# Optimization experiments

Hardware: AMD Instinct MI355X
Metric: run time of the kernel (lower is better)

Reference implementation:

```python
import jax, jax.numpy as jnp
import numpy as np

N = 16384
K = 8

def knn_indices(pos, k):
    # squared pairwise distances via ||a||^2 + ||b||^2 - 2 a.b  -> [N, N]
    sq = jnp.sum(pos * pos, axis=-1)
    d = sq[:, None] + sq[None, :] - 2.0 * (pos @ pos.T)
    n = pos.shape[0]
    d = d.at[jnp.arange(n), jnp.arange(n)].set(jnp.inf)  # exclude self (loop=False)
    _, idx = jax.lax.top_k(-d, k)  # k nearest neighbors per target node
    # PointNetConv adds self-loops by default -> append self index
    return jnp.concatenate([idx, jnp.arange(n)[:, None]], axis=1)  # [N, k+1]

def mlp(x, W1, b1, W2, b2):
    return jax.nn.relu(x @ W1 + b1) @ W2 + b2

def pointnet_conv(x, pos, idx, W1, b1, W2, b2):
    # message: concat(x_j, pos_j - pos_i); aggregate: max over neighbors
    rel = pos[idx] - pos[:, None, :]                 # [N, k+1, 3]
    msg = jnp.concatenate([x[idx], rel], axis=-1)    # [N, k+1, d+3]
    h = mlp(msg, W1, b1, W2, b2)                     # [N, k+1, d_out]
    return jnp.max(h, axis=1)                        # [N, d_out]

def setup_inputs() -> dict:
    key = jax.random.key(0)
    ks = jax.random.split(key, 11)
    def lin(k, fi, fo):
        kw, kb = jax.random.split(k)
        s = 1.0 / np.sqrt(fi)
        return (jax.random.uniform(kw, (fi, fo), jnp.float32, -s, s),
                jax.random.uniform(kb, (fo,), jnp.float32, -s, s))
    W1a, b1a = lin(ks[0], 6, 32)
    W1b, b1b = lin(ks[1], 32, 64)
    W2a, b2a = lin(ks[2], 67, 64)
    W2b, b2b = lin(ks[3], 64, 128)
    Wc, bc = lin(ks[4], 128, 5)
    pos = jax.random.normal(ks[5], (N, 3), jnp.float32)
    return {"pos": pos, "W1a": W1a, "b1a": b1a, "W1b": W1b, "b1b": b1b,
            "W2a": W2a, "b2a": b2a, "W2b": W2b, "b2b": b2b, "Wc": Wc, "bc": bc}

def reference(pos, W1a, b1a, W1b, b1b, W2a, b2a, W2b, b2b, Wc, bc):
    idx = knn_indices(pos, K)                                    # [N, K+1]
    x = jax.nn.relu(pointnet_conv(pos, pos, idx, W1a, b1a, W1b, b1b))  # [N, 64]
    x = jax.nn.relu(pointnet_conv(x, pos, idx, W2a, b2a, W2b, b2b))    # [N, 128]
    logits = x @ Wc + bc                                         # [N, 5]
    return jax.nn.log_softmax(logits, axis=-1)
```

## Files before the change

### kernel.cpp

```cpp
#include <hip/hip_runtime.h>
#include <hip/hip_bf16.h>
#include <math.h>

#define N_PTS 16384
#define KNN 8

#define DT_BF16 1
#define DT_FP32 2

#define WS_FLAG_OFF 0
#define WS_IDX_OFF  64
#define WS_X1_OFF   589888
#define WS_NEEDED   4784192

#define WS_SAT_OFF      (WS_X1_OFF)
#define WS_START_OFF    (WS_X1_OFF + 442368)
#define WS_CURSOR_OFF   (WS_X1_OFF + 884800)
#define WS_PID_OFF      (WS_X1_OFF + 1327168)
#define WS_PTS_OFF      (WS_X1_OFF + 1392704)
#define WS_ROWTOT_OFF   (WS_X1_OFF + 1654848)
#define WS_ROWSTART_OFF (WS_X1_OFF + 1664064)

#define GRID_R   48
#define NROWS2D  (GRID_R * GRID_R)
#define NCELLS   (GRID_R * GRID_R * GRID_R)
#define GLO      -4.5f
#define CELL_E   0.1875f
#define CELL_INV 5.3333335f
#define NBR_MIN  26

__device__ __forceinline__ float bf2f(__hip_bfloat16 v) { return __bfloat162float(v); }

__device__ __forceinline__ float ldf(const float* p, int i) { return p[i]; }
__device__ __forceinline__ float ldf(const __hip_bfloat16* p, int i) { return bf2f(p[i]); }
__device__ __forceinline__ void stf(float* p, int i, float v) { p[i] = v; }
__device__ __forceinline__ void stf(__hip_bfloat16* p, int i, float v) { p[i] = __float2bfloat16(v); }

__device__ __forceinline__ int clamp_idx(int j) {
    return ((unsigned)j < (unsigned)N_PTS) ? j : 0;
}

__device__ __forceinline__ int cell_of(float v) {
    int c = (int)((v - GLO) * CELL_INV);
    return min(max(c, 0), GRID_R - 1);
}

__device__ __forceinline__ int get_dt(const int* flag) {
    return (flag[0] > 16) ? DT_FP32 : DT_BF16;
}

__global__ __launch_bounds__(256) void zero_kernel(int* __restrict__ cnt, int* __restrict__ flag) {
    const int e = blockIdx.x * 256 + threadIdx.x;
    cnt[e] = 0;
    if (e == 0) flag[0] = 0;
}

__global__ __launch_bounds__(256) void sniff_kernel(const unsigned short* __restrict__ posu,
                                                    int* __restrict__ flag) {
    __shared__ int red[256];
    int local = 0;
    for (int e = blockIdx.x * 256 + threadIdx.x; e < 3 * N_PTS; e += 64 * 256) {
        const float v = __uint_as_float(((unsigned)posu[e]) << 16);
        if (!(fabsf(v) <= 64.0f)) local++;
    }
    red[threadIdx.x] = local;
    __syncthreads();
    for (int s = 128; s > 0; s >>= 1) {
        if (threadIdx.x < s) red[threadIdx.x] += red[threadIdx.x + s];
        __syncthreads();
    }
    if (threadIdx.x == 0 && red[0] > 0) atomicAdd(flag, red[0]);
}

template <typename T>
__device__ __forceinline__ void count_body(const T* __restrict__ pos, int* __restrict__ cnt) {
    const int i = blockIdx.x * 256 + threadIdx.x;
    const float x = ldf(pos, 3 * i + 0);
    const float y = ldf(pos, 3 * i + 1);
    const float z = ldf(pos, 3 * i + 2);
    const int c = (cell_of(z) * GRID_R + cell_of(y)) * GRID_R + cell_of(x);
    atomicAdd(&cnt[c], 1);
}

__global__ __launch_bounds__(256) void grid_count_kernel(const void* __restrict__ pos,
                                                         const int* __restrict__ flag,
                                                         int* __restrict__ cnt) {
    if (get_dt(flag) == DT_BF16) count_body<__hip_bfloat16>((const __hip_bfloat16*)pos, cnt);
    else                         count_body<float>((const float*)pos, cnt);
}

__global__ __launch_bounds__(256) void rowscan_kernel(int* __restrict__ sat,
                                                      int* __restrict__ rowtot) {
    const int t = blockIdx.x * 256 + threadIdx.x;
    const int rb = t * GRID_R;
    int acc = 0;
    for (int x = 0; x < GRID_R; ++x) { acc += sat[rb + x]; sat[rb + x] = acc; }
    rowtot[t] = acc;
}

__global__ __launch_bounds__(256) void rowoffset_kernel(const int* __restrict__ rowtot,
                                                        int* __restrict__ rowstart) {
    __shared__ int part[256];
    const int t = threadIdx.x;
    int loc[9]; int s = 0;
#pragma unroll
    for (int k = 0; k < 9; ++k) { loc[k] = rowtot[t * 9 + k]; s += loc[k]; }
    part[t] = s;
    __syncthreads();
    for (int off = 1; off < 256; off <<= 1) {
        int v = (t >= off) ? part[t - off] : 0;
        __syncthreads();
        part[t] += v;
        __syncthreads();
    }
    int run = (t == 0) ? 0 : part[t - 1];
#pragma unroll
    for (int k = 0; k < 9; ++k) { rowstart[t * 9 + k] = run; run += loc[k]; }
}

__global__ __launch_bounds__(256) void cellstart_kernel(const int* __restrict__ satx,
                                                        const int* __restrict__ rowstart,
                                                        int* __restrict__ cstart,
                                                        int* __restrict__ cursor) {
    const int t = blockIdx.x * 256 + threadIdx.x;
    const int rb = t * GRID_R;
    const int base = rowstart[t];
    int prev = 0;
    for (int x = 0; x < GRID_R; ++x) {
        const int v = base + prev;
        cstart[rb + x] = v;
        cursor[rb + x] = v;
        prev = satx[rb + x];
    }
    if (t == NROWS2D - 1) cstart[NCELLS] = base + prev;
}

__global__ __launch_bounds__(256) void saty_kernel(int* __restrict__ sat) {
    const int t = blockIdx.x * 256 + threadIdx.x;
    const int z = t / GRID_R, x = t - z * GRID_R;
    const int base = z * NROWS2D + x;
    int run = 0;
#pragma unroll
    for (int y = 0; y < GRID_R; ++y) {
        run += sat[base + y * GRID_R];
        sat[base + y * GRID_R] = run;
    }
}

__global__ __launch_bounds__(256) void satz_kernel(int* __restrict__ sat) {
    const int t = blockIdx.x * 256 + threadIdx.x;
    int run = 0;
#pragma unroll
    for (int z = 0; z < GRID_R; ++z) {
        run += sat[t + z * NROWS2D];
        sat[t + z * NROWS2D] = run;
    }
}

template <typename T>
__device__ __forceinline__ void scatter_body(const T* __restrict__ pos, int* __restrict__ cursor,
                                             float4* __restrict__ pts4, int* __restrict__ pid) {
    const int i = blockIdx.x * 256 + threadIdx.x;
    const float x = ldf(pos, 3 * i + 0);
    const float y = ldf(pos, 3 * i + 1);
    const float z = ldf(pos, 3 * i + 2);
    const int c = (cell_of(z) * GRID_R + cell_of(y)) * GRID_R + cell_of(x);
    const int slot = atomicAdd(&cursor[c], 1);
    const float sq = fmaf(x, x, fmaf(y, y, z * z));
    pts4[slot] = make_float4(-2.0f * x, -2.0f * y, -2.0f * z, sq);
    pid[slot] = i;
}

__global__ __launch_bounds__(256) void grid_scatter_kernel(const void* __restrict__ pos,
                                                           const int* __restrict__ flag,
                                                           int* __restrict__ cursor,
                                                           float4* __restrict__ pts4,
                                                           int* __restrict__ pid) {
    if (get_dt(flag) == DT_BF16) scatter_body<__hip_bfloat16>((const __hip_bfloat16*)pos, cursor, pts4, pid);
    else                         scatter_body<float>((const float*)pos, cursor, pts4, pid);
}

__device__ __forceinline__ int sat_at(const int* __restrict__ sat, int x, int y, int z) {
    if (x < 0 || y < 0 || z < 0) return 0;
    return sat[(z * GRID_R + y) * GRID_R + x];
}

__device__ __forceinline__ int boxcount(const int* __restrict__ sat,
                                        int x0, int x1, int y0, int y1, int z0, int z1) {
    return sat_at(sat, x1, y1, z1) - sat_at(sat, x0 - 1, y1, z1)
         - sat_at(sat, x1, y0 - 1, z1) - sat_at(sat, x1, y1, z0 - 1)
         + sat_at(sat, x0 - 1, y0 - 1, z1) + sat_at(sat, x0 - 1, y1, z0 - 1)
         + sat_at(sat, x1, y0 - 1, z0 - 1) - sat_at(sat, x0 - 1, y0 - 1, z0 - 1);
}

template <typename T>
__device__ void knn_body(const T* __restrict__ pos,
                         const int* __restrict__ cstart, const int* __restrict__ sat,
                         const float4* __restrict__ pts4, const int* __restrict__ pid,
                         int* __restrict__ idx_out,
                         int* __restrict__ rs, int* __restrict__ epf) {
    const int tid  = threadIdx.x;
    const int lane = tid & 31;
    const int i    = blockIdx.x * 8 + (tid >> 5);

    const float pix = ldf(pos, 3 * i + 0);
    const float piy = ldf(pos, 3 * i + 1);
    const float piz = ldf(pos, 3 * i + 2);
    const float sqi = fmaf(pix, pix, fmaf(piy, piy, piz * piz));
    const int cx = cell_of(pix), cy = cell_of(piy), cz = cell_of(piz);

    float bd[KNN];
    int   bi[KNN];
#pragma unroll
    for (int q = 0; q < KNN; ++q) { bd[q] = INFINITY; bi[q] = 0x7fffffff; }
    float tau = INFINITY;

    auto do_insert = [&](float d, int pj) {
        float cd = d; int ci = pj;
#pragma unroll
        for (int q = 0; q < KNN; ++q) {
            const bool ins = (cd < bd[q]) || (cd == bd[q] && ci < bi[q]);
            const float nd = ins ? cd : bd[q];
            const int   ni = ins ? ci : bi[q];
            const float od = ins ? bd[q] : cd;
            const int   oi = ins ? bi[q] : ci;
            bd[q] = nd; bi[q] = ni; cd = od; ci = oi;
        }
        tau = fminf(tau, bd[KNN - 1]);
    };

    auto scan_win = [&](int rr) {
        const int x0 = max(cx - rr, 0), x1 = min(cx + rr, GRID_R - 1);
        const int y0 = max(cy - rr, 0), y1 = min(cy + rr, GRID_R - 1);
        const int z0 = max(cz - rr, 0), z1 = min(cz + rr, GRID_R - 1);
        const int ny = y1 - y0 + 1;
        const int R  = ny * (z1 - z0 + 1);
        const int xs = x1 - x0 + 1;
        for (int cb = 0; cb < R; cb += 32) {
            const int lr = cb + lane;
            int cnt_r = 0, st_r = 0;
            if (lr < R) {
                const int iz = lr / ny;
                const int iy = lr - iz * ny;
                const int c0 = ((z0 + iz) * GRID_R + (y0 + iy)) * GRID_R + x0;
                st_r  = cstart[c0];
                cnt_r = cstart[c0 + xs] - st_r;
            }
            int pv = cnt_r;
#pragma unroll
            for (int s = 1; s < 32; s <<= 1) {
                const int u = __shfl_up(pv, s, 32);
                if (lane >= s) pv += u;
            }
            const int Mtot = __shfl(pv, 31, 32);
            asm volatile("s_waitcnt lgkmcnt(0)" ::: "memory");
            rs[lane]  = st_r;
            epf[lane] = (lr < R) ? (pv - cnt_r) : 0x7fffffff;
            asm volatile("s_waitcnt lgkmcnt(0)" ::: "memory");
            for (int tb = 0; tb < Mtot; tb += 128) {
                float dls[4]; int pjs[4];
#pragma unroll
                for (int k = 0; k < 4; ++k) {
                    const int t = tb + (k << 5) + lane;
                    dls[k] = INFINITY; pjs[k] = i;
                    if (t < Mtot) {
                        int p = 0;
#pragma unroll
                        for (int st = 16; st >= 1; st >>= 1)
                            if (epf[p + st] <= t) p += st;
                        const int si = rs[p] + (t - epf[p]);
                        const float4 cq = pts4[si];
                        pjs[k] = pid[si];
                        dls[k] = fmaf(cq.x, pix, fmaf(cq.y, piy, fmaf(cq.z, piz, cq.w)));
                    }
                }
#pragma unroll
                for (int k = 0; k < 4; ++k)
                    if (pjs[k] != i && dls[k] <= tau) do_insert(dls[k], pjs[k]);
            }
        }
    };

    float od[KNN];
    int   oi[KNN];
    auto merge_out = [&]() {
#pragma unroll
        for (int k = 0; k < KNN; ++k) {
            float dw = bd[0];
            int   iw = bi[0];
#pragma unroll
            for (int s = 1; s < 32; s <<= 1) {
                const float dx = __shfl_xor(dw, s, 32);
                const int   ix = __shfl_xor(iw, s, 32);
                if (dx < dw || (dx == dw && ix < iw)) { dw = dx; iw = ix; }
            }
            if (bd[0] == dw && bi[0] == iw) {
#pragma unroll
                for (int q = 0; q < KNN - 1; ++q) { bd[q] = bd[q + 1]; bi[q] = bi[q + 1]; }
                bd[KNN - 1] = INFINITY; bi[KNN - 1] = 0x7fffffff;
            }
            od[k] = dw; oi[k] = iw;
        }
    };

    int r;
    {
        const int rl = lane + 1;
        const int bx0 = max(cx - rl, 0), bx1 = min(cx + rl, GRID_R - 1);
        const int by0 = max(cy - rl, 0), by1 = min(cy + rl, GRID_R - 1);
        const int bz0 = max(cz - rl, 0), bz1 = min(cz + rl, GRID_R - 1);
        const int cntl = boxcount(sat, bx0, bx1, by0, by1, bz0, bz1);
        const unsigned long long m = __ballot(cntl >= NBR_MIN);
        const unsigned mh = (unsigned)(m >> (tid & 32));
        r = mh ? (int)__ffs(mh) : 32;
    }

    scan_win(r);

    {
        float mg = INFINITY;
        bool full = true;
        if (cx - r > 0)          { mg = fminf(mg, pix - (GLO + (float)(cx - r) * CELL_E));     full = false; }
        if (cx + r < GRID_R - 1) { mg = fminf(mg, (GLO + (float)(cx + r + 1) * CELL_E) - pix); full = false; }
        if (cy - r > 0)          { mg = fminf(mg, piy - (GLO + (float)(cy - r) * CELL_E));     full = false; }
        if (cy + r < GRID_R - 1) { mg = fminf(mg, (GLO + (float)(cy + r + 1) * CELL_E) - piy); full = false; }
        if (cz - r > 0)          { mg = fminf(mg, piz - (GLO + (float)(cz - r) * CELL_E));     full = false; }
        if (cz + r < GRID_R - 1) { mg = fminf(mg, (GLO + (float)(cz + r + 1) * CELL_E) - piz); full = false; }

        merge_out();
        bool done = full;
        const float d8 = od[KNN - 1];
        if (!full) {
            const float mge  = mg - 1e-5f;
            const float need = mge * mge - sqi;
            done = (d8 < need);
        }

        if (!done) {
            float s2 = sqrtf(fmaxf(d8 + sqi, 0.0f)) + 1e-4f;
            s2 = fminf(s2, 9.0f);
            auto dneed = [&](float frac, int clip) -> int {
                int nd = (int)ceilf((s2 - frac) * CELL_INV);
                nd = max(nd, 0);
                return min(nd, clip);
            };
            const float fxm = pix - (GLO + (float)cx * CELL_E);
            const float fxp = (GLO + (float)(cx + 1) * CELL_E) - pix;
            const float fym = piy - (GLO + (float)cy * CELL_E);
            const float fyp = (GLO + (float)(cy + 1) * CELL_E) - piy;
            const float fzm = piz - (GLO + (float)cz * CELL_E);
            const float fzp = (GLO + (float)(cz + 1) * CELL_E) - piz;
            int r2 = r + 1;
            r2 = max(r2, dneed(fxm, cx));
            r2 = max(r2, dneed(fxp, GRID_R - 1 - cx));
            r2 = max(r2, dneed(fym, cy));
            r2 = max(r2, dneed(fyp, GRID_R - 1 - cy));
            r2 = max(r2, dneed(fzm, cz));
            r2 = max(r2, dneed(fzp, GRID_R - 1 - cz));
            r2 = min(r2, GRID_R);

#pragma unroll
            for (int q = 0; q < KNN; ++q) { bd[q] = INFINITY; bi[q] = 0x7fffffff; }
            tau = d8;
            scan_win(r2);
            merge_out();
        }
    }

    if (lane == 0) {
#pragma unroll
        for (int k = 0; k < KNN; ++k) idx_out[i * 9 + k] = clamp_idx(oi[k]);
        idx_out[i * 9 + 8] = i;
    }
}

__global__ __launch_bounds__(256) void knn_grid_kernel(const void* __restrict__ pos,
                                                       const int* __restrict__ flag,
                                                       const int* __restrict__ cstart,
                                                       const int* __restrict__ sat,
                                                       const float4* __restrict__ pts4,
                                                       const int* __restrict__ pid,
                                                       int* __restrict__ idx_out) {
    __shared__ int rs[8][32];
    __shared__ int epf[8][32];
    const int sg = threadIdx.x >> 5;
    if (get_dt(flag) == DT_BF16)
        knn_body<__hip_bfloat16>((const __hip_bfloat16*)pos, cstart, sat, pts4, pid, idx_out,
                                 rs[sg], epf[sg]);
    else
        knn_body<float>((const float*)pos, cstart, sat, pts4, pid, idx_out, rs[sg], epf[sg]);
}

struct Conv1Smem {
    alignas(16) float wB[32 * 64];
    alignas(16) float h1s[4][9 * 32];
    alignas(16) float wsum[3 * 32];
    alignas(16) float wbot[3 * 32];
    alignas(16) float posn[4][9][3];
    float bA[32];
    float bB[64];
};

template <typename T>
__device__ void conv1_body(const T* __restrict__ pos, const int* __restrict__ idx,
                           const T* __restrict__ W1a, const T* __restrict__ b1a,
                           const T* __restrict__ W1b, const T* __restrict__ b1b,
                           float* __restrict__ x1, Conv1Smem& s) {
    const int tid = threadIdx.x;
    for (int e = tid; e < 96; e += 256) {
        const float bot = ldf(W1a, 96 + e);
        s.wsum[e] = ldf(W1a, e) + bot;
        s.wbot[e] = bot;
    }
    if (tid < 32) s.bA[tid] = ldf(b1a, tid);
    for (int e = tid; e < 2048; e += 256) s.wB[e] = ldf(W1b, e);
    if (tid < 64) s.bB[tid] = ldf(b1b, tid);

    const int tl   = tid >> 6;
    const int lane = tid & 63;
    const int i    = blockIdx.x * 4 + tl;

    if (lane < 27) {
        const int n = lane / 3, c = lane % 3;
        const int j = clamp_idx(idx[i * 9 + n]);
        s.posn[tl][n][c] = ldf(pos, 3 * j + c);
    }
    const float pi0 = ldf(pos, 3 * i + 0);
    const float pi1 = ldf(pos, 3 * i + 1);
    const float pi2 = ldf(pos, 3 * i + 2);
    __syncthreads();

    for (int e = lane; e < 288; e += 64) {
        const int n = e >> 5, k = e & 31;
        float b = fmaf(pi0, s.wbot[k], fmaf(pi1, s.wbot[32 + k], pi2 * s.wbot[64 + k]));
        float v = s.bA[k] - b;
        v = fmaf(s.posn[tl][n][0], s.wsum[k], v);
        v = fmaf(s.posn[tl][n][1], s.wsum[32 + k], v);
        v = fmaf(s.posn[tl][n][2], s.wsum[64 + k], v);
        s.h1s[tl][n * 32 + k] = fmaxf(v, 0.0f);
    }
    __syncthreads();

    float wcol[32];
#pragma unroll
    for (int k = 0; k < 32; ++k) wcol[k] = s.wB[k * 64 + lane];

    float acc = -INFINITY;
    for (int n = 0; n < 9; ++n) {
        float v = s.bB[lane];
#pragma unroll
        for (int k = 0; k < 32; ++k) v = fmaf(s.h1s[tl][n * 32 + k], wcol[k], v);
        acc = fmaxf(acc, v);
    }
    x1[i * 64 + lane] = fmaxf(acc, 0.0f);
}

__global__ __launch_bounds__(256) void conv1_kernel(const void* __restrict__ pos,
                                                    const int* __restrict__ flag,
                                                    const int* __restrict__ idx,
                                                    const void* __restrict__ W1a,
                                                    const void* __restrict__ b1a,
                                                    const void* __restrict__ W1b,
                                                    const void* __restrict__ b1b,
                                                    float* __restrict__ x1) {
    __shared__ Conv1Smem s;
    if (get_dt(flag) == DT_BF16)
        conv1_body<__hip_bfloat16>((const __hip_bfloat16*)pos, idx,
            (const __hip_bfloat16*)W1a, (const __hip_bfloat16*)b1a,
            (const __hip_bfloat16*)W1b, (const __hip_bfloat16*)b1b, x1, s);
    else
        conv1_body<float>((const float*)pos, idx, (const float*)W1a, (const float*)b1a,
            (const float*)W1b, (const float*)b1b, x1, s);
}

struct ZwSmem {
    alignas(16) float wA[67 * 64];
    alignas(16) float xrT[4][68][4];
    float bA[64];
};

template <typename T>
__device__ void zw_body(const T* __restrict__ pos, const T* __restrict__ W2a,
                        const T* __restrict__ b2a, float* __restrict__ x1, ZwSmem& s) {
    const int tid  = threadIdx.x;
    const int wv   = tid >> 6;
    const int lane = tid & 63;
    const int j0   = blockIdx.x * 16 + wv * 4;

    for (int e = tid; e < 4288; e += 256) s.wA[e] = ldf(W2a, e);
    if (tid < 64) s.bA[tid] = ldf(b2a, tid);

#pragma unroll
    for (int p = 0; p < 4; ++p)
        s.xrT[wv][lane][p] = x1[(j0 + p) * 64 + lane];
    if (lane < 12) {
        const int p = lane / 3, c = lane % 3;
        s.xrT[wv][64 + c][p] = ldf(pos, 3 * (j0 + p) + c);
    }
    __syncthreads();

    float a0 = s.bA[lane], a1 = a0, a2 = a0, a3 = a0;
    for (int c = 0; c < 67; ++c) {
        const float w = s.wA[c * 64 + lane];
        const float4 xv = *(const float4*)&s.xrT[wv][c][0];
        a0 = fmaf(xv.x, w, a0);
        a1 = fmaf(xv.y, w, a1);
        a2 = fmaf(xv.z, w, a2);
        a3 = fmaf(xv.w, w, a3);
    }
    x1[(j0 + 0) * 64 + lane] = a0;
    x1[(j0 + 1) * 64 + lane] = a1;
    x1[(j0 + 2) * 64 + lane] = a2;
    x1[(j0 + 3) * 64 + lane] = a3;
}

__global__ __launch_bounds__(256) void zw_kernel(const void* __restrict__ pos,
                                                 const int* __restrict__ flag,
                                                 const void* __restrict__ W2a,
                                                 const void* __restrict__ b2a,
                                                 float* __restrict__ x1) {
    __shared__ ZwSmem s;
    if (get_dt(flag) == DT_BF16)
        zw_body<__hip_bfloat16>((const __hip_bfloat16*)pos, (const __hip_bfloat16*)W2a,
                                (const __hip_bfloat16*)b2a, x1, s);
    else
        zw_body<float>((const float*)pos, (const float*)W2a, (const float*)b2a, x1, s);
}

struct Conv2Smem {
    alignas(16) float h1s[4][9 * 64];
    alignas(16) float row[4][128];
    alignas(16) float wbot[3 * 64];
    alignas(16) float wc[640];
    float bcs[5];
    float sv[4][5];
    int   nb[4][9];
};

template <typename T>
__device__ void conv2_body(const T* __restrict__ pos, const int* __restrict__ idx,
                           const float* __restrict__ zw,
                           const T* __restrict__ W2a, const T* __restrict__ W2b,
                           const T* __restrict__ b2b, const T* __restrict__ Wc,
                           const T* __restrict__ bc, T* __restrict__ out, Conv2Smem& s) {
    const int tid  = threadIdx.x;
    const int l    = tid & 127;
    const int half = tid >> 7;

    float wcol[64];
#pragma unroll
    for (int k = 0; k < 64; ++k) wcol[k] = ldf(W2b, k * 128 + l);
    const float bBl = ldf(b2b, l);

    for (int e = tid; e < 192; e += 256) s.wbot[e] = ldf(W2a, 4096 + e);
    for (int e = tid; e < 640; e += 256) s.wc[e] = ldf(Wc, e);
    if (tid < 5) s.bcs[tid] = ldf(bc, tid);

    const int tl   = tid >> 6;
    const int lane = tid & 63;
    const int i    = blockIdx.x * 4 + tl;

    if (lane < 9) s.nb[tl][lane] = clamp_idx(idx[i * 9 + lane]);
    const float pi0 = ldf(pos, 3 * i + 0);
    const float pi1 = ldf(pos, 3 * i + 1);
    const float pi2 = ldf(pos, 3 * i + 2);
    __syncthreads();

    {
        const float vi = fmaf(pi0, s.wbot[lane], fmaf(pi1, s.wbot[64 + lane], pi2 * s.wbot[128 + lane]));
#pragma unroll
        for (int n = 0; n < 9; ++n) {
            const int j = s.nb[tl][n];
            s.h1s[tl][n * 64 + lane] = fmaxf(zw[j * 64 + lane] - vi, 0.0f);
        }
    }
    __syncthreads();

#pragma unroll
    for (int tt = 0; tt < 2; ++tt) {
        const int tgt = half * 2 + tt;
        float acc = -INFINITY;
        for (int n = 0; n < 9; ++n) {
            float v = bBl;
            for (int k = 0; k < 64; k += 4) {
                const float4 hv = *(const float4*)&s.h1s[tgt][n * 64 + k];
                v = fmaf(hv.x, wcol[k + 0], v);
                v = fmaf(hv.y, wcol[k + 1], v);
                v = fmaf(hv.z, wcol[k + 2], v);
                v = fmaf(hv.w, wcol[k + 3], v);
            }
            acc = fmaxf(acc, v);
        }
        s.row[tgt][l] = fmaxf(acc, 0.0f);
    }
    __syncthreads();

    if (tid < 20) {
        const int tgt = tid / 5, o = tid % 5;
        float v = s.bcs[o];
        for (int k = 0; k < 128; ++k) v = fmaf(s.row[tgt][k], s.wc[k * 5 + o], v);
        s.sv[tgt][o] = v;
    }
    __syncthreads();
    if (tid < 20) {
        const int tgt = tid / 5, o = tid % 5;
        float m = s.sv[tgt][0];
#pragma unroll
        for (int q = 1; q < 5; ++q) m = fmaxf(m, s.sv[tgt][q]);
        float sum = 0.0f;
#pragma unroll
        for (int q = 0; q < 5; ++q) sum += expf(s.sv[tgt][q] - m);
        const float lse = m + logf(sum);
        stf(out, (blockIdx.x * 4 + tgt) * 5 + o, s.sv[tgt][o] - lse);
    }
}

__global__ __launch_bounds__(256) void conv2_head_kernel(const void* __restrict__ pos,
                                                         const int* __restrict__ flag,
                                                         const int* __restrict__ idx,
                                                         const float* __restrict__ zw,
                                                         const void* __restrict__ W2a,
                                                         const void* __restrict__ W2b,
                                                         const void* __restrict__ b2b,
                                                         const void* __restrict__ Wc,
                                                         const void* __restrict__ bc,
                                                         void* __restrict__ out) {
    __shared__ Conv2Smem s;
    if (get_dt(flag) == DT_BF16)
        conv2_body<__hip_bfloat16>((const __hip_bfloat16*)pos, idx, zw,
            (const __hip_bfloat16*)W2a, (const __hip_bfloat16*)W2b, (const __hip_bfloat16*)b2b,
            (const __hip_bfloat16*)Wc, (const __hip_bfloat16*)bc, (__hip_bfloat16*)out, s);
    else
        conv2_body<float>((const float*)pos, idx, zw, (const float*)W2a, (const float*)W2b,
            (const float*)b2b, (const float*)Wc, (const float*)bc, (float*)out, s);
}

extern "C" void kernel_launch(void* const* d_in, const int* in_sizes, int n_in,
                              void* d_out, int out_size, void* d_ws, size_t ws_size,
                              hipStream_t stream) {
    if (ws_size < (size_t)WS_NEEDED) return;

    char* ws = (char*)d_ws;
    int*    flag     = (int*)(ws + WS_FLAG_OFF);
    int*    idx      = (int*)(ws + WS_IDX_OFF);
    float*  x1       = (float*)(ws + WS_X1_OFF);
    int*    sat      = (int*)(ws + WS_SAT_OFF);
    int*    cstart   = (int*)(ws + WS_START_OFF);
    int*    cursor   = (int*)(ws + WS_CURSOR_OFF);
    int*    pid      = (int*)(ws + WS_PID_OFF);
    float4* pts4     = (float4*)(ws + WS_PTS_OFF);
    int*    rowtot   = (int*)(ws + WS_ROWTOT_OFF);
    int*    rowstart = (int*)(ws + WS_ROWSTART_OFF);

    zero_kernel<<<NCELLS / 256, 256, 0, stream>>>(sat, flag);
    sniff_kernel<<<64, 256, 0, stream>>>((const unsigned short*)d_in[0], flag);
    grid_count_kernel<<<N_PTS / 256, 256, 0, stream>>>(d_in[0], flag, sat);
    rowscan_kernel<<<NROWS2D / 256, 256, 0, stream>>>(sat, rowtot);
    rowoffset_kernel<<<1, 256, 0, stream>>>(rowtot, rowstart);
    cellstart_kernel<<<NROWS2D / 256, 256, 0, stream>>>(sat, rowstart, cstart, cursor);
    saty_kernel<<<NROWS2D / 256, 256, 0, stream>>>(sat);
    satz_kernel<<<NROWS2D / 256, 256, 0, stream>>>(sat);
    grid_scatter_kernel<<<N_PTS / 256, 256, 0, stream>>>(d_in[0], flag, cursor, pts4, pid);
    knn_grid_kernel<<<N_PTS / 8, 256, 0, stream>>>(d_in[0], flag, cstart, sat, pts4, pid, idx);
    conv1_kernel<<<N_PTS / 4, 256, 0, stream>>>(d_in[0], flag, idx,
        d_in[1], d_in[2], d_in[3], d_in[4], x1);
    zw_kernel<<<N_PTS / 16, 256, 0, stream>>>(d_in[0], flag, d_in[5], d_in[6], x1);
    conv2_head_kernel<<<N_PTS / 4, 256, 0, stream>>>(d_in[0], flag, idx, x1,
        d_in[5], d_in[7], d_in[8], d_in[9], d_in[10], d_out);
}
```

Before: 244.4 us.

## Fuse grid-build launches, adapt KNN search radius, split FMA accumulator chains

```diff
diff --git a/kernel.cpp b/kernel.cpp
--- a/kernel.cpp
+++ b/kernel.cpp
@@ -20,6 +20,7 @@
 #define WS_PTS_OFF      (WS_X1_OFF + 1392704)
 #define WS_ROWTOT_OFF   (WS_X1_OFF + 1654848)
 #define WS_ROWSTART_OFF (WS_X1_OFF + 1664064)
+#define WS_XPRE_OFF     (WS_X1_OFF + 1673280)
 
 #define GRID_R   48
 #define NROWS2D  (GRID_R * GRID_R)
@@ -28,6 +29,8 @@
 #define CELL_E   0.1875f
 #define CELL_INV 5.3333335f
 #define NBR_MIN  26
+#define NBR_LO   9
+#define M_CAP    768
 
 __device__ __forceinline__ float bf2f(__hip_bfloat16 v) { return __bfloat162float(v); }
 
@@ -90,11 +93,16 @@
 }
 
 __global__ __launch_bounds__(256) void rowscan_kernel(int* __restrict__ sat,
+                                                      int* __restrict__ xpre,
                                                       int* __restrict__ rowtot) {
     const int t = blockIdx.x * 256 + threadIdx.x;
     const int rb = t * GRID_R;
     int acc = 0;
-    for (int x = 0; x < GRID_R; ++x) { acc += sat[rb + x]; sat[rb + x] = acc; }
+    for (int x = 0; x < GRID_R; ++x) {
+        acc += sat[rb + x];
+        sat[rb + x]  = acc;
+        xpre[rb + x] = acc;
+    }
     rowtot[t] = acc;
 }
 
@@ -118,10 +126,11 @@
     for (int k = 0; k < 9; ++k) { rowstart[t * 9 + k] = run; run += loc[k]; }
 }
 
-__global__ __launch_bounds__(256) void cellstart_kernel(const int* __restrict__ satx,
-                                                        const int* __restrict__ rowstart,
-                                                        int* __restrict__ cstart,
-                                                        int* __restrict__ cursor) {
+__global__ __launch_bounds__(256) void cellsaty_kernel(const int* __restrict__ xpre,
+                                                       const int* __restrict__ rowstart,
+                                                       int* __restrict__ cstart,
+                                                       int* __restrict__ cursor,
+                                                       int* __restrict__ sat) {
     const int t = blockIdx.x * 256 + threadIdx.x;
     const int rb = t * GRID_R;
     const int base = rowstart[t];
@@ -130,37 +139,23 @@
         const int v = base + prev;
         cstart[rb + x] = v;
         cursor[rb + x] = v;
-        prev = satx[rb + x];
+        prev = xpre[rb + x];
     }
     if (t == NROWS2D - 1) cstart[NCELLS] = base + prev;
-}
-
-__global__ __launch_bounds__(256) void saty_kernel(int* __restrict__ sat) {
-    const int t = blockIdx.x * 256 + threadIdx.x;
     const int z = t / GRID_R, x = t - z * GRID_R;
-    const int base = z * NROWS2D + x;
+    const int b2 = z * NROWS2D + x;
     int run = 0;
 #pragma unroll
     for (int y = 0; y < GRID_R; ++y) {
-        run += sat[base + y * GRID_R];
-        sat[base + y * GRID_R] = run;
-    }
-}
-
-__global__ __launch_bounds__(256) void satz_kernel(int* __restrict__ sat) {
-    const int t = blockIdx.x * 256 + threadIdx.x;
-    int run = 0;
-#pragma unroll
-    for (int z = 0; z < GRID_R; ++z) {
-        run += sat[t + z * NROWS2D];
-        sat[t + z * NROWS2D] = run;
+        run += sat[b2 + y * GRID_R];
+        sat[b2 + y * GRID_R] = run;
     }
 }
 
 template <typename T>
-__device__ __forceinline__ void scatter_body(const T* __restrict__ pos, int* __restrict__ cursor,
+__device__ __forceinline__ void scatter_body(const T* __restrict__ pos, int i,
+                                             int* __restrict__ cursor,
                                              float4* __restrict__ pts4, int* __restrict__ pid) {
-    const int i = blockIdx.x * 256 + threadIdx.x;
     const float x = ldf(pos, 3 * i + 0);
     const float y = ldf(pos, 3 * i + 1);
     const float z = ldf(pos, 3 * i + 2);
@@ -171,13 +166,25 @@
     pid[slot] = i;
 }
 
-__global__ __launch_bounds__(256) void grid_scatter_kernel(const void* __restrict__ pos,
-                                                           const int* __restrict__ flag,
-                                                           int* __restrict__ cursor,
-                                                           float4* __restrict__ pts4,
-                                                           int* __restrict__ pid) {
-    if (get_dt(flag) == DT_BF16) scatter_body<__hip_bfloat16>((const __hip_bfloat16*)pos, cursor, pts4, pid);
-    else                         scatter_body<float>((const float*)pos, cursor, pts4, pid);
+__global__ __launch_bounds__(256) void satzscatter_kernel(const void* __restrict__ pos,
+                                                          const int* __restrict__ flag,
+                                                          int* __restrict__ sat,
+                                                          int* __restrict__ cursor,
+                                                          float4* __restrict__ pts4,
+                                                          int* __restrict__ pid) {
+    if (blockIdx.x < 9) {
+        const int t = blockIdx.x * 256 + threadIdx.x;
+        int run = 0;
+#pragma unroll
+        for (int z = 0; z < GRID_R; ++z) {
+            run += sat[t + z * NROWS2D];
+            sat[t + z * NROWS2D] = run;
+        }
+    } else {
+        const int i = (blockIdx.x - 9) * 256 + threadIdx.x;
+        if (get_dt(flag) == DT_BF16) scatter_body<__hip_bfloat16>((const __hip_bfloat16*)pos, i, cursor, pts4, pid);
+        else                         scatter_body<float>((const float*)pos, i, cursor, pts4, pid);
+    }
 }
 
 __device__ __forceinline__ int sat_at(const int* __restrict__ sat, int x, int y, int z) {
@@ -310,9 +317,15 @@
         const int by0 = max(cy - rl, 0), by1 = min(cy + rl, GRID_R - 1);
         const int bz0 = max(cz - rl, 0), bz1 = min(cz + rl, GRID_R - 1);
         const int cntl = boxcount(sat, bx0, bx1, by0, by1, bz0, bz1);
-        const unsigned long long m = __ballot(cntl >= NBR_MIN);
-        const unsigned mh = (unsigned)(m >> (tid & 32));
-        r = mh ? (int)__ffs(mh) : 32;
+        const unsigned long long m9  = __ballot(cntl >= NBR_LO);
+        const unsigned long long m26 = __ballot(cntl >= NBR_MIN);
+        const unsigned sh  = (unsigned)(tid & 32);
+        const unsigned mh9  = (unsigned)(m9  >> sh);
+        const unsigned mh26 = (unsigned)(m26 >> sh);
+        const int r9  = mh9  ? (int)__ffs(mh9)  : 32;
+        const int r26 = mh26 ? (int)__ffs(mh26) : 32;
+        const int cnt26 = __shfl(cntl, r26 - 1, 32);
+        r = (cnt26 <= M_CAP) ? r26 : r9;
     }
 
     scan_win(r);
@@ -447,10 +460,15 @@
 
     float acc = -INFINITY;
     for (int n = 0; n < 9; ++n) {
-        float v = s.bB[lane];
-#pragma unroll
-        for (int k = 0; k < 32; ++k) v = fmaf(s.h1s[tl][n * 32 + k], wcol[k], v);
-        acc = fmaxf(acc, v);
+        float s0 = s.bB[lane], s1 = 0.0f, s2 = 0.0f, s3 = 0.0f;
+#pragma unroll
+        for (int k = 0; k < 32; k += 4) {
+            s0 = fmaf(s.h1s[tl][n * 32 + k + 0], wcol[k + 0], s0);
+            s1 = fmaf(s.h1s[tl][n * 32 + k + 1], wcol[k + 1], s1);
+            s2 = fmaf(s.h1s[tl][n * 32 + k + 2], wcol[k + 2], s2);
+            s3 = fmaf(s.h1s[tl][n * 32 + k + 3], wcol[k + 3], s3);
+        }
+        acc = fmaxf(acc, (s0 + s1) + (s2 + s3));
     }
     x1[i * 64 + lane] = fmaxf(acc, 0.0f);
 }
@@ -581,15 +599,31 @@
         const int tgt = half * 2 + tt;
         float acc = -INFINITY;
         for (int n = 0; n < 9; ++n) {
-            float v = bBl;
-            for (int k = 0; k < 64; k += 4) {
-                const float4 hv = *(const float4*)&s.h1s[tgt][n * 64 + k];
-                v = fmaf(hv.x, wcol[k + 0], v);
-                v = fmaf(hv.y, wcol[k + 1], v);
-                v = fmaf(hv.z, wcol[k + 2], v);
-                v = fmaf(hv.w, wcol[k + 3], v);
+            float s0 = bBl, s1 = 0.0f, s2 = 0.0f, s3 = 0.0f;
+#pragma unroll
+            for (int k = 0; k < 64; k += 16) {
+                const float4 h0 = *(const float4*)&s.h1s[tgt][n * 64 + k + 0];
+                const float4 h1 = *(const float4*)&s.h1s[tgt][n * 64 + k + 4];
+                const float4 h2 = *(const float4*)&s.h1s[tgt][n * 64 + k + 8];
+                const float4 h3 = *(const float4*)&s.h1s[tgt][n * 64 + k + 12];
+                s0 = fmaf(h0.x, wcol[k + 0], s0);
+                s0 = fmaf(h0.y, wcol[k + 1], s0);
+                s0 = fmaf(h0.z, wcol[k + 2], s0);
+                s0 = fmaf(h0.w, wcol[k + 3], s0);
+                s1 = fmaf(h1.x, wcol[k + 4], s1);
+                s1 = fmaf(h1.y, wcol[k + 5], s1);
+                s1 = fmaf(h1.z, wcol[k + 6], s1);
+                s1 = fmaf(h1.w, wcol[k + 7], s1);
+                s2 = fmaf(h2.x, wcol[k + 8], s2);
+                s2 = fmaf(h2.y, wcol[k + 9], s2);
+                s2 = fmaf(h2.z, wcol[k + 10], s2);
+                s2 = fmaf(h2.w, wcol[k + 11], s2);
+                s3 = fmaf(h3.x, wcol[k + 12], s3);
+                s3 = fmaf(h3.y, wcol[k + 13], s3);
+                s3 = fmaf(h3.z, wcol[k + 14], s3);
+                s3 = fmaf(h3.w, wcol[k + 15], s3);
             }
-            acc = fmaxf(acc, v);
+            acc = fmaxf(acc, (s0 + s1) + (s2 + s3));
         }
         s.row[tgt][l] = fmaxf(acc, 0.0f);
     }
@@ -651,16 +685,15 @@
     float4* pts4     = (float4*)(ws + WS_PTS_OFF);
     int*    rowtot   = (int*)(ws + WS_ROWTOT_OFF);
     int*    rowstart = (int*)(ws + WS_ROWSTART_OFF);
+    int*    xpre     = (int*)(ws + WS_XPRE_OFF);
 
     zero_kernel<<<NCELLS / 256, 256, 0, stream>>>(sat, flag);
     sniff_kernel<<<64, 256, 0, stream>>>((const unsigned short*)d_in[0], flag);
     grid_count_kernel<<<N_PTS / 256, 256, 0, stream>>>(d_in[0], flag, sat);
-    rowscan_kernel<<<NROWS2D / 256, 256, 0, stream>>>(sat, rowtot);
+    rowscan_kernel<<<NROWS2D / 256, 256, 0, stream>>>(sat, xpre, rowtot);
     rowoffset_kernel<<<1, 256, 0, stream>>>(rowtot, rowstart);
-    cellstart_kernel<<<NROWS2D / 256, 256, 0, stream>>>(sat, rowstart, cstart, cursor);
-    saty_kernel<<<NROWS2D / 256, 256, 0, stream>>>(sat);
-    satz_kernel<<<NROWS2D / 256, 256, 0, stream>>>(sat);
-    grid_scatter_kernel<<<N_PTS / 256, 256, 0, stream>>>(d_in[0], flag, cursor, pts4, pid);
+    cellsaty_kernel<<<NROWS2D / 256, 256, 0, stream>>>(xpre, rowstart, cstart, cursor, sat);
+    satzscatter_kernel<<<9 + N_PTS / 256, 256, 0, stream>>>(d_in[0], flag, sat, cursor, pts4, pid);
     knn_grid_kernel<<<N_PTS / 8, 256, 0, stream>>>(d_in[0], flag, cstart, sat, pts4, pid, idx);
     conv1_kernel<<<N_PTS / 4, 256, 0, stream>>>(d_in[0], flag, idx,
         d_in[1], d_in[2], d_in[3], d_in[4], x1);
```

New measurement: 241.6 us. Within noise of the previous version (-1.1%).
